# Performance work log

Hardware: AMD Instinct MI355X
Metric: run time of the kernel (lower is better)

## Reference

```python
import math
import jax, jax.numpy as jnp
import numpy as np

B, T, D, M, S = 2, 4096, 1024, 256, 8
BEAM = 4
TAU = 1.0


def setup_inputs() -> dict:
    key = jax.random.key(0)
    ks = jax.random.split(key, 24)
    std = 0.02
    inp = {
        "mu": jax.random.normal(ks[0], (B, T, D), jnp.float32),
        "lam": jax.random.uniform(ks[1], (B, T, D), jnp.float32),
        "pi": jax.random.uniform(ks[2], (B, T, 7), jnp.float32),
        "pi_write": jax.random.uniform(ks[3], (B, T, 1), jnp.float32),
        "Wq": jax.random.normal(ks[4], (M, D), jnp.float32) * std,
        "bq": jnp.zeros((M,), jnp.float32),
        "Wk": jax.random.normal(ks[5], (M, D), jnp.float32) * std,
        "bk": jnp.zeros((M,), jnp.float32),
        "Wv": jax.random.normal(ks[6], (M, D), jnp.float32) * std,
        "bv": jnp.zeros((M,), jnp.float32),
        "Wo": jax.random.normal(ks[7], (D, M), jnp.float32) * std,
        "bo": jnp.zeros((D,), jnp.float32),
        "Ws1": jax.random.normal(ks[8], (256, 2 * D + 7), jnp.float32) * std,
        "bs1": jnp.zeros((256,), jnp.float32),
        "Ws2": jax.random.normal(ks[9], (1, 256), jnp.float32) * std,
        "bs2": jnp.zeros((1,), jnp.float32),
        "Wsr": jax.random.normal(ks[10], (M, M), jnp.float32) * std,
        "bsr": jnp.zeros((M,), jnp.float32),
        "scratch_init": jax.random.normal(ks[11], (1, S, M), jnp.float32) * 0.02,
        "gate": jnp.float32(-5.0),
    }
    return inp


def _build_tree(k, v, w):
    """Causal binary tree of weighted span summaries. Level 0 = leaves."""
    levels = [(k, v, w)]
    while k.shape[1] > 1:
        n = k.shape[1]
        if n % 2 == 1:
            pad = ((0, 0), (0, 1), (0, 0))
            k = jnp.pad(k, pad); v = jnp.pad(v, pad); w = jnp.pad(w, pad)
        k1, k2 = k[:, 0::2], k[:, 1::2]
        v1, v2 = v[:, 0::2], v[:, 1::2]
        w1, w2 = w[:, 0::2], w[:, 1::2]
        tw = w1 + w2 + 1e-8
        k = (w1 * k1 + w2 * k2) / tw
        v = (w1 * v1 + w2 * v2) / tw
        w = tw
        levels.append((k, v, w))
    return levels


def _retrieve_at_level(q, keys, values, beam):
    Bq, Tq, Mq = q.shape
    n = keys.shape[1]
    scores = jnp.einsum('btm,bnm->btn', q, keys) / math.sqrt(Mq)
    if n <= Tq:  # causal: query i may only see slot j <= i
        mask = jnp.arange(n)[None, :] > jnp.arange(Tq)[:, None]
        scores = jnp.where(mask[None], -jnp.inf, scores)
    kk = min(beam, n)
    if n > kk:
        vals, idx = jax.lax.top_k(scores, kk)           # (B,T,k)
        p = jax.nn.softmax(vals, axis=-1)               # == softmax of scattered sparse scores
        v_sel = jnp.take_along_axis(values[:, None], idx[..., None], axis=2)  # (B,T,k,M)
        return jnp.einsum('btk,btkm->btm', p, v_sel)
    attn = jax.nn.softmax(scores, axis=-1)
    return jnp.einsum('btn,bnm->btm', attn, values)


def reference(mu, lam, pi, pi_write, Wq, bq, Wk, bk, Wv, bv, Wo, bo,
              Ws1, bs1, Ws2, bs2, Wsr, bsr, scratch_init, gate):
    # ---- write: build causal tree from detached keys/values ----
    mu_d = jax.lax.stop_gradient(mu)
    w0 = jax.lax.stop_gradient(pi_write)                # (B,T,1)
    k = mu_d @ Wk.T + bk
    v = mu_d @ Wv.T + bv
    tree = _build_tree(k, v, w0)

    # ---- read ----
    q = mu @ Wq.T + bq                                  # (B,T,M)
    log_var = -jnp.log(jnp.clip(lam, 1e-6))
    si = jnp.concatenate([mu, log_var, pi], axis=-1)    # (B,T,2D+7)
    h = si @ Ws1.T + bs1
    h = h * jax.nn.sigmoid(h)                           # SiLU
    s = jax.nn.sigmoid((h @ Ws2.T + bs2)[..., 0])       # (B,T)

    scratch = jnp.broadcast_to(scratch_init, (mu.shape[0], S, M))
    sq = q @ Wsr.T + bsr
    sattn = jax.nn.softmax(jnp.einsum('btm,bsm->bts', sq, scratch) / math.sqrt(M), axis=-1)
    scratch_ctx = jnp.einsum('bts,bsm->btm', sattn, scratch)

    level_ctx = [_retrieve_at_level(q, lk, lv, BEAM) for (lk, lv, _) in tree]
    level_stack = jnp.stack(level_ctx, axis=2)          # (B,T,L,M)
    L = level_stack.shape[2]
    level_idx = jnp.arange(L, dtype=mu.dtype)
    s_scaled = s[..., None] * (L - 1)                   # (B,T,1)
    kappa = jnp.exp(-0.5 * ((level_idx - s_scaled) / TAU) ** 2)
    kappa = kappa / jnp.clip(kappa.sum(axis=-1, keepdims=True), 1e-8)
    tree_ctx = jnp.einsum('btl,btlm->btm', kappa, level_stack)

    blend = s[..., None]
    combined = (1.0 - blend) * tree_ctx + blend * scratch_ctx
    out = combined @ Wo.T + bo
    return jax.nn.sigmoid(gate) * out                   # (B,T,D)
```

## Files before the change

kernel.cpp:

```cpp
#include <hip/hip_runtime.h>
#include <math.h>

#define TT 4096
#define BB 2
#define MMDIM 256
#define RTOT 8192
#define NSLICE 39

typedef __attribute__((ext_vector_type(8))) short short8_t;
typedef __attribute__((ext_vector_type(4))) float f32x4;

__device__ __forceinline__ unsigned short f2bf(float x)
{
    unsigned u = __float_as_uint(x);
    u += 0x7fffu + ((u >> 16) & 1u);
    return (unsigned short)(u >> 16);
}

__device__ __forceinline__ void split4(const float* src, unsigned short* hi,
                                       unsigned short* lo, int i)
{
    float4 x = ((const float4*)src)[i];
    ushort4 h, l;
    h.x = f2bf(x.x); l.x = f2bf(x.x - __uint_as_float((unsigned)h.x << 16));
    h.y = f2bf(x.y); l.y = f2bf(x.y - __uint_as_float((unsigned)h.y << 16));
    h.z = f2bf(x.z); l.z = f2bf(x.z - __uint_as_float((unsigned)h.z << 16));
    h.w = f2bf(x.w); l.w = f2bf(x.w - __uint_as_float((unsigned)h.w << 16));
    ((ushort4*)hi)[i] = h;
    ((ushort4*)lo)[i] = l;
}

__global__ __launch_bounds__(256) void gemm_qk_split(
    const float* __restrict__ mu, const float* __restrict__ Wq,
    const float* __restrict__ bq, const float* __restrict__ Wk,
    const float* __restrict__ bk, float* __restrict__ q_, float* __restrict__ k_,
    unsigned short* __restrict__ qkh, unsigned short* __restrict__ qkl,
    const float* __restrict__ Ws1, const float* __restrict__ Wv,
    const float* __restrict__ Wsr, const float* __restrict__ Wo,
    unsigned short* __restrict__ w1h, unsigned short* __restrict__ w1l,
    unsigned short* __restrict__ wvh, unsigned short* __restrict__ wvl,
    unsigned short* __restrict__ wsrh, unsigned short* __restrict__ wsrl,
    unsigned short* __restrict__ woh, unsigned short* __restrict__ wol)
{
    __shared__ float As[2][8][68];
    __shared__ float Ws[2][8][132];
    const int bid = blockIdx.x;
    const int tid = threadIdx.x;

    if (bid >= 512) {
        const int sid = bid - 512;
        if (sid < 256) {
            int r = sid;
            for (int c = tid; c < 2112; c += 256) {
                float v = (c < 2055) ? Ws1[(size_t)r * 2055 + c] : 0.f;
                unsigned short h = f2bf(v);
                w1h[(size_t)r * 2112 + c] = h;
                w1l[(size_t)r * 2112 + c] = f2bf(v - __uint_as_float((unsigned)h << 16));
            }
        } else if (sid < 512) {
            split4(Wv, wvh, wvl, (sid - 256) * 256 + tid);
        } else if (sid < 576) {
            split4(Wsr, wsrh, wsrl, (sid - 512) * 256 + tid);
        } else {
            split4(Wo, woh, wol, (sid - 576) * 256 + tid);
        }
        return;
    }

    const int bx = bid >> 2;
    const int by = bid & 3;
    const int tx = tid & 15;
    const int ty = tid >> 4;
    const int r0 = bx * 64;
    const int c0 = by * 128;
    const bool isq = (c0 < 256);

    const float* W = isq ? (Wq + (size_t)c0 * 1024)
                         : (Wk + (size_t)(c0 - 256) * 1024);
    const float* bias = isq ? (bq + c0) : (bk + (c0 - 256));

    const bool isA = (tid < 128);
    const int sArow = tid >> 1, sAk = (tid & 1) * 4;
    const int sWrow = tid >> 1, sWk = (tid & 1) * 4;

    float acc[4][8] = {};
    float4 rA, rW;

    if (isA) rA = *(const float4*)&mu[(size_t)(r0 + sArow) * 1024 + sAk];
    rW = *(const float4*)&W[(size_t)sWrow * 1024 + sWk];
    if (isA) {
        As[0][sAk + 0][sArow] = rA.x; As[0][sAk + 1][sArow] = rA.y;
        As[0][sAk + 2][sArow] = rA.z; As[0][sAk + 3][sArow] = rA.w;
    }
    Ws[0][sWk + 0][sWrow] = rW.x; Ws[0][sWk + 1][sWrow] = rW.y;
    Ws[0][sWk + 2][sWrow] = rW.z; Ws[0][sWk + 3][sWrow] = rW.w;
    __syncthreads();

    int buf = 0;
    for (int k0 = 0; k0 < 1024; k0 += 8) {
        const bool has = (k0 + 8 < 1024);
        if (has) {
            if (isA) rA = *(const float4*)&mu[(size_t)(r0 + sArow) * 1024 + k0 + 8 + sAk];
            rW = *(const float4*)&W[(size_t)sWrow * 1024 + k0 + 8 + sWk];
        }
        #pragma unroll
        for (int kk = 0; kk < 8; ++kk) {
            float4 a  = *(const float4*)&As[buf][kk][ty * 4];
            float4 b0 = *(const float4*)&Ws[buf][kk][tx * 8];
            float4 b1 = *(const float4*)&Ws[buf][kk][tx * 8 + 4];
            float av[4] = {a.x, a.y, a.z, a.w};
            float bv[8] = {b0.x, b0.y, b0.z, b0.w, b1.x, b1.y, b1.z, b1.w};
            #pragma unroll
            for (int i = 0; i < 4; ++i)
                #pragma unroll
                for (int j = 0; j < 8; ++j)
                    acc[i][j] += av[i] * bv[j];
        }
        if (has) {
            int nb = buf ^ 1;
            if (isA) {
                As[nb][sAk + 0][sArow] = rA.x; As[nb][sAk + 1][sArow] = rA.y;
                As[nb][sAk + 2][sArow] = rA.z; As[nb][sAk + 3][sArow] = rA.w;
            }
            Ws[nb][sWk + 0][sWrow] = rW.x; Ws[nb][sWk + 1][sWrow] = rW.y;
            Ws[nb][sWk + 2][sWrow] = rW.z; Ws[nb][sWk + 3][sWrow] = rW.w;
        }
        __syncthreads();
        buf ^= 1;
    }

    const int lcol = (c0 & 255) + tx * 8;
    #pragma unroll
    for (int i = 0; i < 4; ++i) {
        int row = r0 + ty * 4 + i;
        float o[8];
        #pragma unroll
        for (int j = 0; j < 8; ++j) o[j] = acc[i][j] + bias[tx * 8 + j];
        float* dst = isq ? &q_[(size_t)row * MMDIM + lcol]
                         : &k_[(size_t)row * MMDIM + lcol];
        *(float4*)dst       = make_float4(o[0], o[1], o[2], o[3]);
        *(float4*)(dst + 4) = make_float4(o[4], o[5], o[6], o[7]);
        size_t srow = isq ? (size_t)row : (size_t)(RTOT + row);
        short8_t sh, sl;
        #pragma unroll
        for (int j = 0; j < 8; ++j) {
            unsigned short h = f2bf(o[j]);
            sh[j] = (short)h;
            sl[j] = (short)f2bf(o[j] - __uint_as_float((unsigned)h << 16));
        }
        *(short8_t*)&qkh[srow * MMDIM + lcol] = sh;
        *(short8_t*)&qkl[srow * MMDIM + lcol] = sl;
    }
}

template<int ASRC, int WITH_GATE>
__device__ __forceinline__ void gemm_mfma_body(
    unsigned short (*Ah)[72], unsigned short (*Al)[72],
    unsigned short (*Bh)[72], unsigned short (*Bl)[72],
    const float* __restrict__ A, const float* __restrict__ lam,
    const float* __restrict__ pi,
    const unsigned short* __restrict__ Wh, const unsigned short* __restrict__ Wl,
    const float* __restrict__ bias, const float* __restrict__ gate,
    float* __restrict__ C, int K, int N, int bx, int by)
{
    const int tid = threadIdx.x;
    const int lane = tid & 63;
    const int wv = tid >> 6;
    const int r0 = bx * 64;
    const int c0 = by * 128;

    f32x4 acc0[8] = {}, acc1[8] = {}, acc2[8] = {};

    const int arow = wv * 16 + (lane & 15);
    const int koff = (lane >> 4) * 8;

    for (int kc = 0; kc < K; kc += 64) {
        #pragma unroll
        for (int i = 0; i < 2; ++i) {
            int g = tid + i * 256;
            int row = g >> 3, gq = g & 7;
            float x[8];
            if (ASRC == 0) {
                float4 v0 = *(const float4*)&A[(size_t)(r0 + row) * K + kc + gq * 8];
                float4 v1 = *(const float4*)&A[(size_t)(r0 + row) * K + kc + gq * 8 + 4];
                x[0] = v0.x; x[1] = v0.y; x[2] = v0.z; x[3] = v0.w;
                x[4] = v1.x; x[5] = v1.y; x[6] = v1.z; x[7] = v1.w;
            } else {
                #pragma unroll
                for (int e = 0; e < 8; ++e) {
                    int c = kc + gq * 8 + e;
                    float val;
                    if (c < 1024)      val = A[(size_t)(r0 + row) * 1024 + c];
                    else if (c < 2048) val = -logf(fmaxf(lam[(size_t)(r0 + row) * 1024 + (c - 1024)], 1e-6f));
                    else if (c < 2055) val = pi[(size_t)(r0 + row) * 7 + (c - 2048)];
                    else               val = 0.f;
                    x[e] = val;
                }
            }
            short8_t sh, sl;
            #pragma unroll
            for (int e = 0; e < 8; ++e) {
                unsigned short h = f2bf(x[e]);
                sh[e] = (short)h;
                sl[e] = (short)f2bf(x[e] - __uint_as_float((unsigned)h << 16));
            }
            *(short8_t*)&Ah[row][gq * 8] = sh;
            *(short8_t*)&Al[row][gq * 8] = sl;
        }
        #pragma unroll
        for (int i = 0; i < 4; ++i) {
            int g = tid + i * 256;
            int row = g >> 3, gq = g & 7;
            *(short8_t*)&Bh[row][gq * 8] = *(const short8_t*)&Wh[(size_t)(c0 + row) * K + kc + gq * 8];
            *(short8_t*)&Bl[row][gq * 8] = *(const short8_t*)&Wl[(size_t)(c0 + row) * K + kc + gq * 8];
        }
        __syncthreads();
        #pragma unroll
        for (int kt = 0; kt < 2; ++kt) {
            short8_t afh = *(const short8_t*)&Ah[arow][kt * 32 + koff];
            short8_t afl = *(const short8_t*)&Al[arow][kt * 32 + koff];
            #pragma unroll
            for (int ct = 0; ct < 8; ++ct) {
                short8_t bh = *(const short8_t*)&Bh[ct * 16 + (lane & 15)][kt * 32 + koff];
                short8_t bl = *(const short8_t*)&Bl[ct * 16 + (lane & 15)][kt * 32 + koff];
                acc0[ct] = __builtin_amdgcn_mfma_f32_16x16x32_bf16(afh, bh, acc0[ct], 0, 0, 0);
                acc1[ct] = __builtin_amdgcn_mfma_f32_16x16x32_bf16(afl, bh, acc1[ct], 0, 0, 0);
                acc2[ct] = __builtin_amdgcn_mfma_f32_16x16x32_bf16(afh, bl, acc2[ct], 0, 0, 0);
            }
        }
        __syncthreads();
    }

    float g = 1.f;
    if (WITH_GATE) g = 1.f / (1.f + expf(-gate[0]));
    #pragma unroll
    for (int ct = 0; ct < 8; ++ct) {
        int col = c0 + ct * 16 + (lane & 15);
        float b = bias[col];
        #pragma unroll
        for (int r = 0; r < 4; ++r) {
            int row = r0 + wv * 16 + (lane >> 4) * 4 + r;
            C[(size_t)row * N + col] = (acc0[ct][r] + acc1[ct][r] + acc2[ct][r] + b) * g;
        }
    }
}

template<int ASRC, int WITH_GATE>
__global__ __launch_bounds__(256) void gemm_mfma(
    const float* __restrict__ A, const float* __restrict__ lam,
    const float* __restrict__ pi,
    const unsigned short* __restrict__ Wh, const unsigned short* __restrict__ Wl,
    const float* __restrict__ bias, const float* __restrict__ gate,
    float* __restrict__ C, int K, int N)
{
    __shared__ unsigned short Ah[64][72], Al[64][72];
    __shared__ unsigned short Bh[128][72], Bl[128][72];
    gemm_mfma_body<ASRC, WITH_GATE>(Ah, Al, Bh, Bl, A, lam, pi, Wh, Wl,
                                    bias, gate, C, K, N, blockIdx.x, blockIdx.y);
}

__global__ __launch_bounds__(256) void gemm_vh(
    const float* __restrict__ mu, const float* __restrict__ lam,
    const float* __restrict__ pi,
    const unsigned short* __restrict__ wvh, const unsigned short* __restrict__ wvl,
    const float* __restrict__ bv,
    const unsigned short* __restrict__ w1h, const unsigned short* __restrict__ w1l,
    const float* __restrict__ bs1,
    float* __restrict__ v_, float* __restrict__ h_)
{
    __shared__ unsigned short Ah[64][72], Al[64][72];
    __shared__ unsigned short Bh[128][72], Bl[128][72];
    if (blockIdx.y < 2)
        gemm_mfma_body<0, 0>(Ah, Al, Bh, Bl, mu, nullptr, nullptr, wvh, wvl,
                             bv, nullptr, v_, 1024, 256, blockIdx.x, blockIdx.y);
    else
        gemm_mfma_body<1, 0>(Ah, Al, Bh, Bl, mu, lam, pi, w1h, w1l,
                             bs1, nullptr, h_, 2112, 256, blockIdx.x, blockIdx.y - 2);
}

__global__ __launch_bounds__(256) void s_scratch_kernel(
    const float* __restrict__ h, const float* __restrict__ Ws2,
    const float* __restrict__ bs2, const float* __restrict__ sq,
    const float* __restrict__ scr, float* __restrict__ kap,
    float* __restrict__ ctx)
{
    const int tid = threadIdx.x;
    const int wave = tid >> 6, lane = tid & 63;
    const int t = blockIdx.x * 4 + wave;

    float4 hv = *(const float4*)&h[(size_t)t * MMDIM + lane * 4];
    float4 wv = *(const float4*)&Ws2[lane * 4];
    float p = 0.f;
    p += (hv.x / (1.f + expf(-hv.x))) * wv.x;
    p += (hv.y / (1.f + expf(-hv.y))) * wv.y;
    p += (hv.z / (1.f + expf(-hv.z))) * wv.z;
    p += (hv.w / (1.f + expf(-hv.w))) * wv.w;
    #pragma unroll
    for (int o = 32; o; o >>= 1) p += __shfl_xor(p, o);

    float z = p + bs2[0];
    float s = 1.f / (1.f + expf(-z));
    float c = s * 12.f;
    float Z = 0.f;
    #pragma unroll
    for (int l = 0; l < 13; ++l) {
        float d = (float)l - c;
        Z += expf(-0.5f * d * d);
    }
    Z = fmaxf(Z, 1e-8f);
    if (lane < 13) {
        float d = (float)lane - c;
        kap[(size_t)t * 16 + lane] = (1.f - s) * expf(-0.5f * d * d) / Z;
    }

    float4 qv = *(const float4*)&sq[(size_t)t * MMDIM + lane * 4];
    float4 fr[8];
    float sc[8];
    #pragma unroll
    for (int ss = 0; ss < 8; ++ss) {
        fr[ss] = *(const float4*)&scr[ss * MMDIM + lane * 4];
        sc[ss] = qv.x * fr[ss].x + qv.y * fr[ss].y + qv.z * fr[ss].z + qv.w * fr[ss].w;
    }
    #pragma unroll
    for (int ss = 0; ss < 8; ++ss) {
        #pragma unroll
        for (int o = 32; o; o >>= 1) sc[ss] += __shfl_xor(sc[ss], o);
        sc[ss] *= 0.0625f;
    }
    float mx = sc[0];
    #pragma unroll
    for (int ss = 1; ss < 8; ++ss) mx = fmaxf(mx, sc[ss]);
    float sum = 0.f;
    #pragma unroll
    for (int ss = 0; ss < 8; ++ss) { sc[ss] = expf(sc[ss] - mx); sum += sc[ss]; }
    float inv = 1.f / sum;
    float4 o = {0, 0, 0, 0};
    #pragma unroll
    for (int ss = 0; ss < 8; ++ss) {
        float pp = sc[ss] * inv;
        o.x += pp * fr[ss].x; o.y += pp * fr[ss].y;
        o.z += pp * fr[ss].z; o.w += pp * fr[ss].w;
    }
    o.x *= s; o.y *= s; o.z *= s; o.w *= s;
    *(float4*)&ctx[(size_t)t * MMDIM + lane * 4] = o;
}

__global__ __launch_bounds__(256) void tree_all(
    const float* __restrict__ kleaf, const float* __restrict__ vleaf,
    const float* __restrict__ pw, float* __restrict__ wl6,
    float* __restrict__ kt_, float* __restrict__ vt_,
    unsigned short* __restrict__ kth, unsigned short* __restrict__ ktl)
{
    __shared__ float kb[254][64];
    __shared__ float vb[254][64];
    __shared__ float wl[254];
    const int tid = threadIdx.x;
    const int g  = blockIdx.x >> 2;
    const int mc = blockIdx.x & 3;
    const int b  = blockIdx.y;
    const int wb = b * 4095;

    for (int idx = tid; idx < 128 * 64; idx += 256) {
        int j = idx >> 6, m = idx & 63;
        size_t gi = ((size_t)b * TT + g * 128 + j) * MMDIM + mc * 64 + m;
        kb[j][m] = kleaf[gi];
        vb[j][m] = vleaf[gi];
    }
    if (tid < 128) wl[tid] = pw[b * 4096 + g * 128 + tid];
    __syncthreads();

    int pb = 0, cb = 128;
    for (int l = 1; l <= 6; ++l) {
        int nloc = 128 >> l;
        int offl = TT - (8192 >> l);
        int gbase = g * nloc;
        if (tid < nloc)
            wl[cb + tid] = wl[pb + 2 * tid] + wl[pb + 2 * tid + 1] + 1e-8f;
        __syncthreads();
        for (int idx = tid; idx < nloc * 64; idx += 256) {
            int j = idx >> 6, m = idx & 63;
            float w1 = wl[pb + 2 * j];
            float w2 = wl[pb + 2 * j + 1];
            float tw = wl[cb + j];
            float kvv = (w1 * kb[pb + 2 * j][m] + w2 * kb[pb + 2 * j + 1][m]) / tw;
            float vvv = (w1 * vb[pb + 2 * j][m] + w2 * vb[pb + 2 * j + 1][m]) / tw;
            kb[cb + j][m] = kvv;
            vb[cb + j][m] = vvv;
            size_t go = (size_t)(wb + offl + gbase + j) * MMDIM + mc * 64 + m;
            kt_[go] = kvv;
            vt_[go] = vvv;
            unsigned short hh = f2bf(kvv);
            kth[go] = hh;
            ktl[go] = f2bf(kvv - __uint_as_float((unsigned)hh << 16));
        }
        __syncthreads();
        pb = cb; cb += nloc;
    }
    if (mc == 0 && tid < 2) wl6[b * 64 + g * 2 + tid] = wl[pb + tid];
}

__global__ __launch_bounds__(256) void tree_deep(
    float* __restrict__ kt_, float* __restrict__ vt_,
    const float* __restrict__ wl6,
    unsigned short* __restrict__ kth, unsigned short* __restrict__ ktl)
{
    __shared__ float kb[128][68];
    __shared__ float vb[128][68];
    __shared__ float wl[127];
    const int tid = threadIdx.x;
    const int mc = blockIdx.x;
    const int b = blockIdx.y;
    const int wb = b * 4095;

    for (int idx = tid; idx < 64 * 64; idx += 256) {
        int j = idx >> 6, m = idx & 63;
        size_t gi = (size_t)(wb + 3968 + j) * MMDIM + mc * 64 + m;
        kb[j][m] = kt_[gi];
        vb[j][m] = vt_[gi];
    }
    if (tid < 64) wl[tid] = wl6[b * 64 + tid];
    __syncthreads();

    int pb = 0;
    int pbw = 0, cbw = 64;
    for (int l = 7; l <= 12; ++l) {
        int nout = 4096 >> l;
        int cb = 128 - (128 >> (l - 6));
        int offl = TT - (8192 >> l);
        if (tid < nout)
            wl[cbw + tid] = wl[pbw + 2 * tid] + wl[pbw + 2 * tid + 1] + 1e-8f;
        __syncthreads();
        for (int idx = tid; idx < nout * 64; idx += 256) {
            int j = idx >> 6, m = idx & 63;
            float w1 = wl[pbw + 2 * j];
            float w2 = wl[pbw + 2 * j + 1];
            float tw = wl[cbw + j];
            float kvv = (w1 * kb[pb + 2 * j][m] + w2 * kb[pb + 2 * j + 1][m]) / tw;
            float vvv = (w1 * vb[pb + 2 * j][m] + w2 * vb[pb + 2 * j + 1][m]) / tw;
            kb[cb + j][m] = kvv;
            vb[cb + j][m] = vvv;
            size_t go = (size_t)(wb + offl + j) * MMDIM + mc * 64 + m;
            kt_[go] = kvv;
            vt_[go] = vvv;
            unsigned short hh = f2bf(kvv);
            kth[go] = hh;
            ktl[go] = f2bf(kvv - __uint_as_float((unsigned)hh << 16));
        }
        __syncthreads();
        pb = cb;
        pbw = cbw; cbw += nout;
    }
}

__device__ __forceinline__ unsigned long long pack_key(float v, int col)
{
    unsigned u = __float_as_uint(v);
    u ^= ((unsigned)((int)u >> 31)) | 0x80000000u;
    return ((unsigned long long)u << 32) | (unsigned)(~col);
}

__device__ __forceinline__ void unpack_key(unsigned long long k, float& v, int& col)
{
    unsigned u = (unsigned)(k >> 32);
    u ^= (u & 0x80000000u) ? 0x80000000u : 0xFFFFFFFFu;
    v = __uint_as_float(u);
    col = (int)(~(unsigned)k);
}

__device__ __forceinline__ unsigned long long shfl_xor_u64(unsigned long long v, int off)
{
    int lo = __shfl_xor((int)(unsigned)v, off);
    int hi = __shfl_xor((int)(v >> 32), off);
    return ((unsigned long long)(unsigned)hi << 32) | (unsigned)lo;
}

__device__ __forceinline__ void ins4u(unsigned long long k, unsigned long long t[4])
{
    if (k <= t[3]) return;
    t[3] = k;
    if (t[3] > t[2]) { unsigned long long x = t[2]; t[2] = t[3]; t[3] = x; }
    if (t[2] > t[1]) { unsigned long long x = t[1]; t[1] = t[2]; t[2] = x; }
    if (t[1] > t[0]) { unsigned long long x = t[0]; t[0] = t[1]; t[1] = x; }
}

__device__ __forceinline__ void ins5u(unsigned long long k, unsigned long long t[5])
{
    if (k <= t[4]) return;
    t[4] = k;
    if (t[4] > t[3]) { unsigned long long x = t[3]; t[3] = t[4]; t[4] = x; }
    if (t[3] > t[2]) { unsigned long long x = t[2]; t[2] = t[3]; t[3] = x; }
    if (t[2] > t[1]) { unsigned long long x = t[1]; t[1] = t[2]; t[2] = x; }
    if (t[1] > t[0]) { unsigned long long x = t[0]; t[0] = t[1]; t[1] = x; }
}

__device__ __forceinline__ bool beats(float v, int id, float v2, int id2)
{
    return (v > v2) || (v == v2 && id < id2);
}

__device__ __forceinline__ void ins5(float v, int id, float tv[5], int ti[5])
{
    if (!beats(v, id, tv[4], ti[4])) return;
    tv[4] = v; ti[4] = id;
    #pragma unroll
    for (int s = 4; s > 0; --s) {
        if (beats(tv[s], ti[s], tv[s - 1], ti[s - 1])) {
            float fv = tv[s]; tv[s] = tv[s - 1]; tv[s - 1] = fv;
            int iv = ti[s]; ti[s] = ti[s - 1]; ti[s - 1] = iv;
        }
    }
}

__device__ __forceinline__ void slice_map(int sid, int& level, int& c0)
{
    if (sid < 16)      { level = 0; c0 = sid << 8; }
    else if (sid < 24) { level = 1; c0 = (sid - 16) << 8; }
    else if (sid < 28) { level = 2; c0 = (sid - 24) << 8; }
    else if (sid < 30) { level = 3; c0 = (sid - 28) << 8; }
    else               { level = sid - 26; c0 = 0; }
}

__global__ __launch_bounds__(256) void topk_mfma(
    const unsigned short* __restrict__ qkh, const unsigned short* __restrict__ qkl,
    const unsigned short* __restrict__ kth, const unsigned short* __restrict__ ktl,
    float2* __restrict__ topw)
{
    __shared__ unsigned short kbh[32][264];
    __shared__ unsigned short kbl[32][264];

    const int tid = threadIdx.x;
    const int lane = tid & 63;
    const int wv = tid >> 6;
    const int r0 = blockIdx.x * 64;
    const int sid = blockIdx.y;
    const int b = r0 >> 12;
    const int t0 = r0 & 4095;

    int level, c0b;
    slice_map(sid, level, c0b);
    const int n = TT >> level;
    const int nv = min(min(n, t0 + 64), c0b + 256);

    if (c0b >= nv) {
        if (tid < 64) {
            float2 e = make_float2(-INFINITY, __int_as_float(0x7fffffff));
            #pragma unroll
            for (int s = 0; s < 5; ++s)
                topw[(size_t)(sid * 5 + s) * RTOT + r0 + tid] = e;
        }
        return;
    }

    const unsigned short* Kh;
    const unsigned short* Kl;
    if (level == 0) {
        Kh = qkh + (size_t)RTOT * MMDIM + (size_t)b * TT * MMDIM;
        Kl = qkl + (size_t)RTOT * MMDIM + (size_t)b * TT * MMDIM;
    } else {
        size_t off = (size_t)b * 4095 + (TT - (8192 >> level));
        Kh = kth + off * MMDIM;
        Kl = ktl + off * MMDIM;
    }

    const int arow = r0 + wv * 16 + (lane & 15);
    const int koff = (lane >> 4) * 8;
    short8_t ah[8], al[8];
    #pragma unroll
    for (int kt = 0; kt < 8; ++kt) {
        ah[kt] = *(const short8_t*)(qkh + (size_t)arow * MMDIM + kt * 32 + koff);
        al[kt] = *(const short8_t*)(qkl + (size_t)arow * MMDIM + kt * 32 + koff);
    }

    unsigned long long tk[4][4] = {};
    const int trow0 = t0 + wv * 16 + (lane >> 4) * 4;

    const int scol = tid >> 3;
    const int kseg = (tid & 7) * 32;

    for (int c0 = c0b; c0 < nv; c0 += 32) {
        {
            int cc = min(c0 + scol, n - 1);
            const unsigned short* gh = Kh + (size_t)cc * MMDIM + kseg;
            const unsigned short* gl = Kl + (size_t)cc * MMDIM + kseg;
            #pragma unroll
            for (int i = 0; i < 4; ++i) {
                *(short8_t*)&kbh[scol][kseg + i * 8] = *(const short8_t*)(gh + i * 8);
                *(short8_t*)&kbl[scol][kseg + i * 8] = *(const short8_t*)(gl + i * 8);
            }
        }
        __syncthreads();

        #pragma unroll
        for (int ct = 0; ct < 2; ++ct) {
            f32x4 a0 = {0.f, 0.f, 0.f, 0.f};
            f32x4 a1 = {0.f, 0.f, 0.f, 0.f};
            f32x4 a2 = {0.f, 0.f, 0.f, 0.f};
            const int bc = ct * 16 + (lane & 15);
            #pragma unroll
            for (int kt = 0; kt < 8; ++kt) {
                short8_t bh = *(const short8_t*)&kbh[bc][kt * 32 + koff];
                short8_t bl = *(const short8_t*)&kbl[bc][kt * 32 + koff];
                a0 = __builtin_amdgcn_mfma_f32_16x16x32_bf16(ah[kt], bh, a0, 0, 0, 0);
                a1 = __builtin_amdgcn_mfma_f32_16x16x32_bf16(al[kt], bh, a1, 0, 0, 0);
                a2 = __builtin_amdgcn_mfma_f32_16x16x32_bf16(ah[kt], bl, a2, 0, 0, 0);
            }
            const int col = c0 + bc;
            #pragma unroll
            for (int r = 0; r < 4; ++r) {
                float sc = (a0[r] + a1[r] + a2[r]) * 0.0625f;
                unsigned long long key =
                    (col <= trow0 + r && col < n) ? pack_key(sc, col) : 0ull;
                if (__any(key > tk[r][3])) ins4u(key, tk[r]);
            }
        }
        __syncthreads();
    }

    #pragma unroll
    for (int r = 0; r < 4; ++r) {
        unsigned long long k5[5];
        #pragma unroll
        for (int s = 0; s < 4; ++s) k5[s] = tk[r][s];
        k5[4] = 0ull;
        #pragma unroll
        for (int pass = 0; pass < 4; ++pass) {
            int off = 1 << pass;
            unsigned long long o[5];
            #pragma unroll
            for (int s = 0; s < 5; ++s) o[s] = shfl_xor_u64(k5[s], off);
            #pragma unroll
            for (int s = 0; s < 5; ++s) ins5u(o[s], k5);
        }
        if ((lane & 15) == 0) {
            int row = r0 + wv * 16 + (lane >> 4) * 4 + r;
            #pragma unroll
            for (int s = 0; s < 5; ++s) {
                float2 e;
                if (k5[s] == 0ull) {
                    e = make_float2(-INFINITY, __int_as_float(0x7fffffff));
                } else {
                    float v; int c;
                    unpack_key(k5[s], v, c);
                    e = make_float2(v, __int_as_float(c));
                }
                topw[(size_t)(sid * 5 + s) * RTOT + row] = e;
            }
        }
    }
}

__global__ __launch_bounds__(256) void merge_gather(
    const float2* __restrict__ topw, const float* __restrict__ q,
    const float* __restrict__ kl0, const float* __restrict__ ktf,
    const float* __restrict__ vl0, const float* __restrict__ vtree,
    const float* __restrict__ kap, float* __restrict__ ctx)
{
    const int tid = threadIdx.x;
    const int lane = tid & 63;
    const int wv = __builtin_amdgcn_readfirstlane(tid >> 6);
    const int row = blockIdx.x * 4 + wv;
    const int b = row >> 12;

    float cr[4] = {0, 0, 0, 0};
    const float4 q4 = *(const float4*)&q[(size_t)row * MMDIM + lane * 4];

    for (int l = 0; l <= 12; ++l) {
        int s0, cnt;
        if (l == 0)      { s0 = 0;  cnt = 16; }
        else if (l == 1) { s0 = 16; cnt = 8; }
        else if (l == 2) { s0 = 24; cnt = 4; }
        else if (l == 3) { s0 = 28; cnt = 2; }
        else             { s0 = 26 + l; cnt = 1; }

        float tv[5]; int ti[5];
        #pragma unroll
        for (int s = 0; s < 5; ++s) { tv[s] = -INFINITY; ti[s] = 0x7fffffff; }
        for (int sl = 0; sl < cnt; ++sl) {
            #pragma unroll
            for (int s = 0; s < 5; ++s) {
                float2 e = topw[(size_t)((s0 + sl) * 5 + s) * RTOT + row];
                if (e.x > -INFINITY) ins5(e.x, __float_as_int(e.y), tv, ti);
            }
        }

        const float* Kf = (l == 0)
            ? kl0 + (size_t)b * TT * MMDIM
            : ktf + ((size_t)b * 4095 + (TT - (8192 >> l))) * MMDIM;

        bool ambig = (l <= 9) && (tv[3] - tv[4] < 1e-4f);
        if (ambig) {
            float rv[5]; int ri[5];
            #pragma unroll
            for (int s = 0; s < 5; ++s) { rv[s] = -INFINITY; ri[s] = 0x7fffffff; }
            for (int sl = 0; sl < cnt; ++sl) {
                #pragma unroll
                for (int s = 0; s < 5; ++s) {
                    float2 e = topw[(size_t)((s0 + sl) * 5 + s) * RTOT + row];
                    if (e.x > -INFINITY) {
                        int idx = __float_as_int(e.y);
                        float4 k4 = *(const float4*)&Kf[(size_t)idx * MMDIM + lane * 4];
                        float p = q4.x * k4.x + q4.y * k4.y + q4.z * k4.z + q4.w * k4.w;
                        #pragma unroll
                        for (int o = 32; o; o >>= 1) p += __shfl_xor(p, o);
                        ins5(p * 0.0625f, idx, rv, ri);
                    }
                }
            }
            #pragma unroll
            for (int s = 0; s < 5; ++s) { tv[s] = rv[s]; ti[s] = ri[s]; }
        }

        float m0 = tv[0];
        float e0 = expf(tv[0] - m0);
        float e1 = expf(tv[1] - m0);
        float e2 = expf(tv[2] - m0);
        float e3 = expf(tv[3] - m0);
        float sum = e0 + e1 + e2 + e3;
        float kp = kap[(size_t)row * 16 + l];
        float scl = kp / sum;
        float ps[4] = {e0 * scl, e1 * scl, e2 * scl, e3 * scl};

        const float* Vb = (l == 0)
            ? vl0 + (size_t)b * TT * MMDIM
            : vtree + ((size_t)b * 4095 + (TT - (8192 >> l))) * MMDIM;

        #pragma unroll
        for (int s = 0; s < 4; ++s) {
            if (ps[s] > 0.f) {
                float4 vv = *(const float4*)&Vb[(size_t)ti[s] * MMDIM + lane * 4];
                cr[0] += ps[s] * vv.x; cr[1] += ps[s] * vv.y;
                cr[2] += ps[s] * vv.z; cr[3] += ps[s] * vv.w;
            }
        }
    }

    float* cp = ctx + (size_t)row * MMDIM + lane * 4;
    float4 c = *(float4*)cp;
    c.x += cr[0]; c.y += cr[1]; c.z += cr[2]; c.w += cr[3];
    *(float4*)cp = c;
}

extern "C" void kernel_launch(void* const* d_in, const int* in_sizes, int n_in,
                              void* d_out, int out_size, void* d_ws, size_t ws_size,
                              hipStream_t stream)
{
    const float* mu  = (const float*)d_in[0];
    const float* lam = (const float*)d_in[1];
    const float* pi  = (const float*)d_in[2];
    const float* pw  = (const float*)d_in[3];
    const float* Wq  = (const float*)d_in[4];
    const float* bq  = (const float*)d_in[5];
    const float* Wk  = (const float*)d_in[6];
    const float* bk  = (const float*)d_in[7];
    const float* Wv  = (const float*)d_in[8];
    const float* bv  = (const float*)d_in[9];
    const float* Wo  = (const float*)d_in[10];
    const float* bo  = (const float*)d_in[11];
    const float* Ws1 = (const float*)d_in[12];
    const float* bs1 = (const float*)d_in[13];
    const float* Ws2 = (const float*)d_in[14];
    const float* bs2 = (const float*)d_in[15];
    const float* Wsr = (const float*)d_in[16];
    const float* bsr = (const float*)d_in[17];
    const float* scr = (const float*)d_in[18];
    const float* gate = (const float*)d_in[19];
    float* out = (float*)d_out;

    float* w = (float*)d_ws;
    const size_t RM = (size_t)RTOT * MMDIM;
    float* q_   = w;  w += RM;
    float* k_   = w;  w += RM;
    float* v_   = w;  w += RM;
    float* h_   = w;  w += RM;
    float* sq_  = w;  w += RM;
    float* ctx_ = w;  w += RM;
    float* sb_  = w;  w += RTOT;
    float* kap_ = w;  w += (size_t)RTOT * 16;
    float* kt_  = w;  w += (size_t)BB * 4095 * MMDIM;
    float* vt_  = w;  w += (size_t)BB * 4095 * MMDIM;
    float* wl6_ = w;  w += (size_t)BB * 4095;
    unsigned short* qkh_ = (unsigned short*)w;  w += RM;
    unsigned short* qkl_ = (unsigned short*)w;  w += RM;
    unsigned short* kth_ = (unsigned short*)w;  w += (size_t)BB * 4095 * MMDIM / 2;
    unsigned short* ktl_ = (unsigned short*)w;  w += (size_t)BB * 4095 * MMDIM / 2;
    float2* topw = (float2*)w;  w += (size_t)NSLICE * 5 * RTOT * 2;
    unsigned short* w1h_ = (unsigned short*)w;  w += (size_t)256 * 2112 / 2;
    unsigned short* w1l_ = (unsigned short*)w;  w += (size_t)256 * 2112 / 2;
    unsigned short* wvh_ = (unsigned short*)w;  w += (size_t)256 * 1024 / 2;
    unsigned short* wvl_ = (unsigned short*)w;  w += (size_t)256 * 1024 / 2;
    unsigned short* wsrh_ = (unsigned short*)w; w += (size_t)256 * 256 / 2;
    unsigned short* wsrl_ = (unsigned short*)w; w += (size_t)256 * 256 / 2;
    unsigned short* woh_ = (unsigned short*)w;  w += (size_t)1024 * 256 / 2;
    unsigned short* wol_ = (unsigned short*)w;  w += (size_t)1024 * 256 / 2;
    (void)sb_;

    gemm_qk_split<<<1344, 256, 0, stream>>>(mu, Wq, bq, Wk, bk, q_, k_,
                                            qkh_, qkl_, Ws1, Wv, Wsr, Wo,
                                            w1h_, w1l_, wvh_, wvl_,
                                            wsrh_, wsrl_, woh_, wol_);

    gemm_vh<<<dim3(128, 4), 256, 0, stream>>>(mu, lam, pi, wvh_, wvl_, bv,
                                              w1h_, w1l_, bs1, v_, h_);
    gemm_mfma<0, 0><<<dim3(128, 2), 256, 0, stream>>>(q_, nullptr, nullptr, wsrh_, wsrl_,
                                                      bsr, nullptr, sq_, 256, 256);
    s_scratch_kernel<<<2048, 256, 0, stream>>>(h_, Ws2, bs2, sq_, scr, kap_, ctx_);

    tree_all<<<dim3(128, BB), 256, 0, stream>>>(k_, v_, pw, wl6_, kt_, vt_,
                                                kth_, ktl_);
    tree_deep<<<dim3(4, BB), 256, 0, stream>>>(kt_, vt_, wl6_, kth_, ktl_);

    topk_mfma<<<dim3(128, NSLICE), 256, 0, stream>>>(qkh_, qkl_, kth_, ktl_, topw);
    merge_gather<<<2048, 256, 0, stream>>>(topw, q_, k_, kt_, v_, vt_, kap_, ctx_);
    gemm_mfma<0, 1><<<dim3(128, 8), 256, 0, stream>>>(ctx_, nullptr, nullptr, woh_, wol_,
                                                      bo, gate, out, 256, 1024);
}
```

Before: 720.4 us.

## Merge independent stages into heterogeneous fused launches and split top-k by slice

Combines the V/h projection GEMMs, the scratch-query GEMM and the key-tree build into one launch, with each block index range dispatching to a different body. A second launch runs the leaf-level top-k slices (which score against leaf keys in qk) alongside the s/scratch computation and the value-tree build. The remaining tree-level top-k slices run in a separate kernel after tree_deep. The aim is fewer launches and barriers and better overlap of independent work. In exchange, the fused kernels allocate the largest shared memory any branch needs, which may reduce occupancy for the lighter branches.

```diff
diff --git a/kernel.cpp b/kernel.cpp
--- a/kernel.cpp
+++ b/kernel.cpp
@@ -259,112 +259,22 @@
                                     bias, gate, C, K, N, blockIdx.x, blockIdx.y);
 }
 
-__global__ __launch_bounds__(256) void gemm_vh(
-    const float* __restrict__ mu, const float* __restrict__ lam,
-    const float* __restrict__ pi,
-    const unsigned short* __restrict__ wvh, const unsigned short* __restrict__ wvl,
-    const float* __restrict__ bv,
-    const unsigned short* __restrict__ w1h, const unsigned short* __restrict__ w1l,
-    const float* __restrict__ bs1,
-    float* __restrict__ v_, float* __restrict__ h_)
-{
-    __shared__ unsigned short Ah[64][72], Al[64][72];
-    __shared__ unsigned short Bh[128][72], Bl[128][72];
-    if (blockIdx.y < 2)
-        gemm_mfma_body<0, 0>(Ah, Al, Bh, Bl, mu, nullptr, nullptr, wvh, wvl,
-                             bv, nullptr, v_, 1024, 256, blockIdx.x, blockIdx.y);
-    else
-        gemm_mfma_body<1, 0>(Ah, Al, Bh, Bl, mu, lam, pi, w1h, w1l,
-                             bs1, nullptr, h_, 2112, 256, blockIdx.x, blockIdx.y - 2);
-}
-
-__global__ __launch_bounds__(256) void s_scratch_kernel(
-    const float* __restrict__ h, const float* __restrict__ Ws2,
-    const float* __restrict__ bs2, const float* __restrict__ sq,
-    const float* __restrict__ scr, float* __restrict__ kap,
-    float* __restrict__ ctx)
-{
+template<int IS_K>
+__device__ __forceinline__ void tree16_body(
+    char* smem, const float* __restrict__ leaf, const float* __restrict__ pw,
+    float* __restrict__ wl6, float* __restrict__ tout,
+    unsigned short* __restrict__ th, unsigned short* __restrict__ tl,
+    int x, int b)
+{
+    float (*kb)[64] = (float(*)[64])smem;
+    float* wl = (float*)(smem + 254 * 64 * 4);
     const int tid = threadIdx.x;
-    const int wave = tid >> 6, lane = tid & 63;
-    const int t = blockIdx.x * 4 + wave;
-
-    float4 hv = *(const float4*)&h[(size_t)t * MMDIM + lane * 4];
-    float4 wv = *(const float4*)&Ws2[lane * 4];
-    float p = 0.f;
-    p += (hv.x / (1.f + expf(-hv.x))) * wv.x;
-    p += (hv.y / (1.f + expf(-hv.y))) * wv.y;
-    p += (hv.z / (1.f + expf(-hv.z))) * wv.z;
-    p += (hv.w / (1.f + expf(-hv.w))) * wv.w;
-    #pragma unroll
-    for (int o = 32; o; o >>= 1) p += __shfl_xor(p, o);
-
-    float z = p + bs2[0];
-    float s = 1.f / (1.f + expf(-z));
-    float c = s * 12.f;
-    float Z = 0.f;
-    #pragma unroll
-    for (int l = 0; l < 13; ++l) {
-        float d = (float)l - c;
-        Z += expf(-0.5f * d * d);
-    }
-    Z = fmaxf(Z, 1e-8f);
-    if (lane < 13) {
-        float d = (float)lane - c;
-        kap[(size_t)t * 16 + lane] = (1.f - s) * expf(-0.5f * d * d) / Z;
-    }
-
-    float4 qv = *(const float4*)&sq[(size_t)t * MMDIM + lane * 4];
-    float4 fr[8];
-    float sc[8];
-    #pragma unroll
-    for (int ss = 0; ss < 8; ++ss) {
-        fr[ss] = *(const float4*)&scr[ss * MMDIM + lane * 4];
-        sc[ss] = qv.x * fr[ss].x + qv.y * fr[ss].y + qv.z * fr[ss].z + qv.w * fr[ss].w;
-    }
-    #pragma unroll
-    for (int ss = 0; ss < 8; ++ss) {
-        #pragma unroll
-        for (int o = 32; o; o >>= 1) sc[ss] += __shfl_xor(sc[ss], o);
-        sc[ss] *= 0.0625f;
-    }
-    float mx = sc[0];
-    #pragma unroll
-    for (int ss = 1; ss < 8; ++ss) mx = fmaxf(mx, sc[ss]);
-    float sum = 0.f;
-    #pragma unroll
-    for (int ss = 0; ss < 8; ++ss) { sc[ss] = expf(sc[ss] - mx); sum += sc[ss]; }
-    float inv = 1.f / sum;
-    float4 o = {0, 0, 0, 0};
-    #pragma unroll
-    for (int ss = 0; ss < 8; ++ss) {
-        float pp = sc[ss] * inv;
-        o.x += pp * fr[ss].x; o.y += pp * fr[ss].y;
-        o.z += pp * fr[ss].z; o.w += pp * fr[ss].w;
-    }
-    o.x *= s; o.y *= s; o.z *= s; o.w *= s;
-    *(float4*)&ctx[(size_t)t * MMDIM + lane * 4] = o;
-}
-
-__global__ __launch_bounds__(256) void tree_all(
-    const float* __restrict__ kleaf, const float* __restrict__ vleaf,
-    const float* __restrict__ pw, float* __restrict__ wl6,
-    float* __restrict__ kt_, float* __restrict__ vt_,
-    unsigned short* __restrict__ kth, unsigned short* __restrict__ ktl)
-{
-    __shared__ float kb[254][64];
-    __shared__ float vb[254][64];
-    __shared__ float wl[254];
-    const int tid = threadIdx.x;
-    const int g  = blockIdx.x >> 2;
-    const int mc = blockIdx.x & 3;
-    const int b  = blockIdx.y;
+    const int g = x >> 2, mc = x & 3;
     const int wb = b * 4095;
 
     for (int idx = tid; idx < 128 * 64; idx += 256) {
         int j = idx >> 6, m = idx & 63;
-        size_t gi = ((size_t)b * TT + g * 128 + j) * MMDIM + mc * 64 + m;
-        kb[j][m] = kleaf[gi];
-        vb[j][m] = vleaf[gi];
+        kb[j][m] = leaf[((size_t)b * TT + g * 128 + j) * MMDIM + mc * 64 + m];
     }
     if (tid < 128) wl[tid] = pw[b * 4096 + g * 128 + tid];
     __syncthreads();
@@ -382,21 +292,130 @@
             float w1 = wl[pb + 2 * j];
             float w2 = wl[pb + 2 * j + 1];
             float tw = wl[cb + j];
-            float kvv = (w1 * kb[pb + 2 * j][m] + w2 * kb[pb + 2 * j + 1][m]) / tw;
-            float vvv = (w1 * vb[pb + 2 * j][m] + w2 * vb[pb + 2 * j + 1][m]) / tw;
-            kb[cb + j][m] = kvv;
-            vb[cb + j][m] = vvv;
+            float val = (w1 * kb[pb + 2 * j][m] + w2 * kb[pb + 2 * j + 1][m]) / tw;
+            kb[cb + j][m] = val;
             size_t go = (size_t)(wb + offl + gbase + j) * MMDIM + mc * 64 + m;
-            kt_[go] = kvv;
-            vt_[go] = vvv;
-            unsigned short hh = f2bf(kvv);
-            kth[go] = hh;
-            ktl[go] = f2bf(kvv - __uint_as_float((unsigned)hh << 16));
+            tout[go] = val;
+            if (IS_K) {
+                unsigned short hh = f2bf(val);
+                th[go] = hh;
+                tl[go] = f2bf(val - __uint_as_float((unsigned)hh << 16));
+            }
         }
         __syncthreads();
         pb = cb; cb += nloc;
     }
-    if (mc == 0 && tid < 2) wl6[b * 64 + g * 2 + tid] = wl[pb + tid];
+    if (IS_K && mc == 0 && tid < 2) wl6[b * 64 + g * 2 + tid] = wl[pb + tid];
+}
+
+__global__ __launch_bounds__(256) void fused_proj(
+    const float* __restrict__ mu, const float* __restrict__ lam,
+    const float* __restrict__ pi,
+    const unsigned short* __restrict__ wvh, const unsigned short* __restrict__ wvl,
+    const float* __restrict__ bv,
+    const unsigned short* __restrict__ w1h, const unsigned short* __restrict__ w1l,
+    const float* __restrict__ bs1,
+    const unsigned short* __restrict__ wsrh, const unsigned short* __restrict__ wsrl,
+    const float* __restrict__ bsr,
+    const float* __restrict__ q_, float* __restrict__ v_, float* __restrict__ h_,
+    float* __restrict__ sq_,
+    const float* __restrict__ k_, const float* __restrict__ pw,
+    float* __restrict__ wl6, float* __restrict__ kt_,
+    unsigned short* __restrict__ kth, unsigned short* __restrict__ ktl)
+{
+    __shared__ char smem[66048];
+    const int bid = blockIdx.x;
+
+    if (bid < 768) {
+        unsigned short (*Ah)[72] = (unsigned short(*)[72])smem;
+        unsigned short (*Al)[72] = (unsigned short(*)[72])(smem + 9216);
+        unsigned short (*Bh)[72] = (unsigned short(*)[72])(smem + 18432);
+        unsigned short (*Bl)[72] = (unsigned short(*)[72])(smem + 36864);
+        if (bid < 512) {
+            int bx = bid & 127, by = bid >> 7;
+            if (by < 2)
+                gemm_mfma_body<0, 0>(Ah, Al, Bh, Bl, mu, nullptr, nullptr,
+                                     wvh, wvl, bv, nullptr, v_, 1024, 256, bx, by);
+            else
+                gemm_mfma_body<1, 0>(Ah, Al, Bh, Bl, mu, lam, pi,
+                                     w1h, w1l, bs1, nullptr, h_, 2112, 256, bx, by - 2);
+        } else {
+            int t = bid - 512;
+            gemm_mfma_body<0, 0>(Ah, Al, Bh, Bl, q_, nullptr, nullptr,
+                                 wsrh, wsrl, bsr, nullptr, sq_, 256, 256,
+                                 t & 127, t >> 7);
+        }
+    } else {
+        int t = bid - 768;
+        tree16_body<1>(smem, k_, pw, wl6, kt_, kth, ktl, t & 127, t >> 7);
+    }
+}
+
+__device__ __forceinline__ void s_scratch_body(
+    int bx, const float* __restrict__ h, const float* __restrict__ Ws2,
+    const float* __restrict__ bs2, const float* __restrict__ sq,
+    const float* __restrict__ scr, float* __restrict__ kap,
+    float* __restrict__ ctx)
+{
+    const int tid = threadIdx.x;
+    const int wave = tid >> 6, lane = tid & 63;
+    const int t = bx * 4 + wave;
+
+    float4 hv = *(const float4*)&h[(size_t)t * MMDIM + lane * 4];
+    float4 wv = *(const float4*)&Ws2[lane * 4];
+    float p = 0.f;
+    p += (hv.x / (1.f + expf(-hv.x))) * wv.x;
+    p += (hv.y / (1.f + expf(-hv.y))) * wv.y;
+    p += (hv.z / (1.f + expf(-hv.z))) * wv.z;
+    p += (hv.w / (1.f + expf(-hv.w))) * wv.w;
+    #pragma unroll
+    for (int o = 32; o; o >>= 1) p += __shfl_xor(p, o);
+
+    float z = p + bs2[0];
+    float s = 1.f / (1.f + expf(-z));
+    float c = s * 12.f;
+    float Z = 0.f;
+    #pragma unroll
+    for (int l = 0; l < 13; ++l) {
+        float d = (float)l - c;
+        Z += expf(-0.5f * d * d);
+    }
+    Z = fmaxf(Z, 1e-8f);
+    if (lane < 13) {
+        float d = (float)lane - c;
+        kap[(size_t)t * 16 + lane] = (1.f - s) * expf(-0.5f * d * d) / Z;
+    }
+
+    float4 qv = *(const float4*)&sq[(size_t)t * MMDIM + lane * 4];
+    float4 fr[8];
+    float sc[8];
+    #pragma unroll
+    for (int ss = 0; ss < 8; ++ss) {
+        fr[ss] = *(const float4*)&scr[ss * MMDIM + lane * 4];
+        sc[ss] = qv.x * fr[ss].x + qv.y * fr[ss].y + qv.z * fr[ss].z + qv.w * fr[ss].w;
+    }
+    #pragma unroll
+    for (int ss = 0; ss < 8; ++ss) {
+        #pragma unroll
+        for (int o = 32; o; o >>= 1) sc[ss] += __shfl_xor(sc[ss], o);
+        sc[ss] *= 0.0625f;
+    }
+    float mx = sc[0];
+    #pragma unroll
+    for (int ss = 1; ss < 8; ++ss) mx = fmaxf(mx, sc[ss]);
+    float sum = 0.f;
+    #pragma unroll
+    for (int ss = 0; ss < 8; ++ss) { sc[ss] = expf(sc[ss] - mx); sum += sc[ss]; }
+    float inv = 1.f / sum;
+    float4 o = {0, 0, 0, 0};
+    #pragma unroll
+    for (int ss = 0; ss < 8; ++ss) {
+        float pp = sc[ss] * inv;
+        o.x += pp * fr[ss].x; o.y += pp * fr[ss].y;
+        o.z += pp * fr[ss].z; o.w += pp * fr[ss].w;
+    }
+    o.x *= s; o.y *= s; o.z *= s; o.w *= s;
+    *(float4*)&ctx[(size_t)t * MMDIM + lane * 4] = o;
 }
 
 __global__ __launch_bounds__(256) void tree_deep(
@@ -520,19 +539,19 @@
     else               { level = sid - 26; c0 = 0; }
 }
 
-__global__ __launch_bounds__(256) void topk_mfma(
+__device__ __forceinline__ void topk_body(
+    char* smem,
     const unsigned short* __restrict__ qkh, const unsigned short* __restrict__ qkl,
     const unsigned short* __restrict__ kth, const unsigned short* __restrict__ ktl,
-    float2* __restrict__ topw)
-{
-    __shared__ unsigned short kbh[32][264];
-    __shared__ unsigned short kbl[32][264];
+    float2* __restrict__ topw, int rg, int sid)
+{
+    unsigned short (*kbh)[264] = (unsigned short(*)[264])smem;
+    unsigned short (*kbl)[264] = (unsigned short(*)[264])(smem + 16896);
 
     const int tid = threadIdx.x;
     const int lane = tid & 63;
     const int wv = tid >> 6;
-    const int r0 = blockIdx.x * 64;
-    const int sid = blockIdx.y;
+    const int r0 = rg * 64;
     const int b = r0 >> 12;
     const int t0 = r0 & 4095;
 
@@ -647,6 +666,38 @@
             }
         }
     }
+}
+
+__global__ __launch_bounds__(256) void fused_mid(
+    const unsigned short* __restrict__ qkh, const unsigned short* __restrict__ qkl,
+    float2* __restrict__ topw,
+    const float* __restrict__ h_, const float* __restrict__ Ws2,
+    const float* __restrict__ bs2, const float* __restrict__ sq_,
+    const float* __restrict__ scr, float* __restrict__ kap_,
+    float* __restrict__ ctx_,
+    const float* __restrict__ v_, const float* __restrict__ pw,
+    float* __restrict__ vt_)
+{
+    __shared__ char smem[66048];
+    const int bid = blockIdx.x;
+    if (bid < 2048) {
+        topk_body(smem, qkh, qkl, qkh, qkl, topw, bid & 127, bid >> 7);
+    } else if (bid < 4096) {
+        s_scratch_body(bid - 2048, h_, Ws2, bs2, sq_, scr, kap_, ctx_);
+    } else {
+        int t = bid - 4096;
+        tree16_body<0>(smem, v_, pw, nullptr, vt_, nullptr, nullptr,
+                       t & 127, t >> 7);
+    }
+}
+
+__global__ __launch_bounds__(256) void topk_rest(
+    const unsigned short* __restrict__ qkh, const unsigned short* __restrict__ qkl,
+    const unsigned short* __restrict__ kth, const unsigned short* __restrict__ ktl,
+    float2* __restrict__ topw)
+{
+    __shared__ char smem[33792];
+    topk_body(smem, qkh, qkl, kth, ktl, topw, blockIdx.x, 16 + blockIdx.y);
 }
 
 __global__ __launch_bounds__(256) void merge_gather(
@@ -799,17 +850,18 @@
                                             w1h_, w1l_, wvh_, wvl_,
                                             wsrh_, wsrl_, woh_, wol_);
 
-    gemm_vh<<<dim3(128, 4), 256, 0, stream>>>(mu, lam, pi, wvh_, wvl_, bv,
-                                              w1h_, w1l_, bs1, v_, h_);
-    gemm_mfma<0, 0><<<dim3(128, 2), 256, 0, stream>>>(q_, nullptr, nullptr, wsrh_, wsrl_,
-                                                      bsr, nullptr, sq_, 256, 256);
-    s_scratch_kernel<<<2048, 256, 0, stream>>>(h_, Ws2, bs2, sq_, scr, kap_, ctx_);
-
-    tree_all<<<dim3(128, BB), 256, 0, stream>>>(k_, v_, pw, wl6_, kt_, vt_,
-                                                kth_, ktl_);
+    fused_proj<<<1024, 256, 0, stream>>>(mu, lam, pi, wvh_, wvl_, bv,
+                                         w1h_, w1l_, bs1, wsrh_, wsrl_, bsr,
+                                         q_, v_, h_, sq_,
+                                         k_, pw, wl6_, kt_, kth_, ktl_);
+
+    fused_mid<<<4352, 256, 0, stream>>>(qkh_, qkl_, topw, h_, Ws2, bs2,
+                                        sq_, scr, kap_, ctx_, v_, pw, vt_);
+
     tree_deep<<<dim3(4, BB), 256, 0, stream>>>(kt_, vt_, wl6_, kth_, ktl_);
 
-    topk_mfma<<<dim3(128, NSLICE), 256, 0, stream>>>(qkh_, qkl_, kth_, ktl_, topw);
+    topk_rest<<<dim3(128, 23), 256, 0, stream>>>(qkh_, qkl_, kth_, ktl_, topw);
+
     merge_gather<<<2048, 256, 0, stream>>>(topw, q_, k_, kt_, v_, vt_, kap_, ctx_);
     gemm_mfma<0, 1><<<dim3(128, 8), 256, 0, stream>>>(ctx_, nullptr, nullptr, woh_, wol_,
                                                       bo, gate, out, 256, 1024);
```

Result: slower. 749.5 us (+4.0%).
